# Kernel optimization log

Hardware: AMD Instinct MI355X
Metric: run time of the kernel (lower is better)

## Reference

```python
import jax, jax.numpy as jnp
import numpy as np

N_NODES = 100000
N_EDGES = 3200000  # avg degree 32
NFEAT = 512
NOUT = 7
DIMS = [NFEAT, 12, 10, 8, 6, 4, NOUT]  # hard-coded hidden widths from __init__


def setup_inputs() -> dict:
    key = jax.random.key(0)
    ks = jax.random.split(key, 4 + 2 * 6)
    inp = {
        "x": jax.random.normal(ks[0], (N_NODES, NFEAT), dtype=jnp.float32),
        "edge_val": jax.random.uniform(ks[1], (N_EDGES,), dtype=jnp.float32) / 32.0,  # ~normalized adj
        "edge_src": jax.random.randint(ks[2], (N_EDGES,), 0, N_NODES),
        "edge_dst": jax.random.randint(ks[3], (N_EDGES,), 0, N_NODES),
    }
    for i in range(6):
        s = 1.0 / np.sqrt(DIMS[i + 1])  # pygcn reset_parameters: U(-1/sqrt(out), 1/sqrt(out))
        inp[f"W{i+1}"] = jax.random.uniform(ks[4 + 2 * i], (DIMS[i], DIMS[i + 1]), jnp.float32, -s, s)
        inp[f"b{i+1}"] = jax.random.uniform(ks[5 + 2 * i], (DIMS[i + 1],), jnp.float32, -s, s)
    return inp


def reference(x, edge_val, W1, b1, W2, b2, W3, b3, W4, b4, W5, b5, W6, b6,
              edge_src, edge_dst):
    n = x.shape[0]

    def gc(h, W, b):
        s = h @ W                                   # [N, out] dense mm
        m = edge_val[:, None] * s[edge_src]         # gather + scale per edge
        agg = jax.ops.segment_sum(m, edge_dst, num_segments=n)  # spmm scatter
        return agg + b

    tanhshrink = lambda v: v - jnp.tanh(v)

    h = gc(x, W1, b1)                # dropout p=0 -> identity
    h = jax.nn.relu(gc(h, W2, b2))   # eval-mode dropout -> identity
    h = tanhshrink(gc(h, W3, b3))
    h = tanhshrink(gc(h, W4, b4))
    h = gc(h, W5, b5)
    return gc(h, W6, b6)
```

## Files before the change

### kernel.cpp

```cpp
#include <hip/hip_runtime.h>
#include <hip/hip_bf16.h>
#include <math.h>
#include <stdint.h>


#define T_EDGES 12800
#define NB_MAX  1600
#define FCAP    2560

__global__ __launch_bounds__(256) void hist_kernel(const int* __restrict__ dst,
                                                   int* __restrict__ ghist, int E, int NB) {
    __shared__ int h[NB_MAX];
    for (int i = threadIdx.x; i < NB; i += 256) h[i] = 0;
    __syncthreads();
    int base = blockIdx.x * T_EDGES;
    int n = min(T_EDGES, E - base);
    for (int i = threadIdx.x; i < n; i += 256)
        atomicAdd(&h[((unsigned)dst[base + i]) >> 6], 1);
    __syncthreads();
    for (int i = threadIdx.x; i < NB; i += 256)
        ghist[(size_t)blockIdx.x * NB + i] = h[i];
}

__global__ __launch_bounds__(256) void scanA_kernel(const int* __restrict__ ghist,
                                                    int* __restrict__ btot, int NT, int NB) {
    __shared__ int red[256];
    int b = blockIdx.x, t = threadIdx.x;
    int s = 0;
    for (int tt = t; tt < NT; tt += 256) s += ghist[(size_t)tt * NB + b];
    red[t] = s;
    __syncthreads();
    for (int off = 128; off > 0; off >>= 1) {
        if (t < off) red[t] += red[t + off];
        __syncthreads();
    }
    if (t == 0) btot[b] = red[0];
}

__global__ __launch_bounds__(256) void scanB_kernel(const int* __restrict__ btot,
                                                    int* __restrict__ bbase,
                                                    int* __restrict__ bucket_ptr, int NB) {
    __shared__ int part[256];
    int t = threadIdx.x;
    int chunk = (NB + 255) / 256;
    int lo = t * chunk, hi = min(lo + chunk, NB);
    int s = 0;
    for (int i = lo; i < hi; i++) s += btot[i];
    part[t] = s;
    __syncthreads();
    for (int off = 1; off < 256; off <<= 1) {
        int x = (t >= off) ? part[t - off] : 0;
        __syncthreads();
        part[t] += x;
        __syncthreads();
    }
    int run = part[t] - s;
    for (int i = lo; i < hi; i++) {
        bbase[i] = run;
        bucket_ptr[i] = run;
        run += btot[i];
    }
    if (t == 255) bucket_ptr[NB] = run;
}

__global__ __launch_bounds__(256) void scanC_kernel(const int* __restrict__ ghist,
                                                    const int* __restrict__ bbase,
                                                    int* __restrict__ goff, int NT, int NB) {
    __shared__ int part[256];
    int b = blockIdx.x, t = threadIdx.x;
    int v = (t < NT) ? ghist[(size_t)t * NB + b] : 0;
    part[t] = v;
    __syncthreads();
    for (int off = 1; off < 256; off <<= 1) {
        int x = (t >= off) ? part[t - off] : 0;
        __syncthreads();
        part[t] += x;
        __syncthreads();
    }
    if (t < NT) goff[(size_t)t * NB + b] = bbase[b] + part[t] - v;
}

__global__ __launch_bounds__(256) void scatter_kernel(const int* __restrict__ src,
                                                      const int* __restrict__ dst,
                                                      const float* __restrict__ val,
                                                      const int* __restrict__ ghist,
                                                      const int* __restrict__ goff,
                                                      int2* __restrict__ edges, int E, int NB) {
    __shared__ unsigned perm[T_EDGES];
    __shared__ int loff[NB_MAX];
    __shared__ int lcur[NB_MAX];
    __shared__ int part[256];
    int tb = blockIdx.x, t = threadIdx.x;
    int base = tb * T_EDGES;
    int n = min(T_EDGES, E - base);

    int chunk = (NB + 255) / 256;
    int lo = t * chunk, hi = min(lo + chunk, NB);
    int s = 0;
    for (int i = lo; i < hi; i++) {
        int c = ghist[(size_t)tb * NB + i];
        loff[i] = c;
        s += c;
    }
    part[t] = s;
    __syncthreads();
    for (int off = 1; off < 256; off <<= 1) {
        int x = (t >= off) ? part[t - off] : 0;
        __syncthreads();
        part[t] += x;
        __syncthreads();
    }
    int run = part[t] - s;
    for (int i = lo; i < hi; i++) {
        int c = loff[i];
        loff[i] = run;
        lcur[i] = run;
        run += c;
    }
    __syncthreads();

    for (int i = t; i < n; i += 256) {
        int d = dst[base + i];
        unsigned b = ((unsigned)d) >> 6;
        int p = atomicAdd(&lcur[b], 1);
        perm[p] = (unsigned)i | (b << 14) | ((unsigned)(d & 63) << 25);
    }
    __syncthreads();

    for (int o = t; o < n; o += 256) {
        unsigned v = perm[o];
        int li = v & 16383;
        int b  = (v >> 14) & 2047;
        int ld = v >> 25;
        int g  = goff[(size_t)tb * NB + b] + (o - loff[b]);
        edges[g] = make_int2(src[base + li] | (ld << 17), __float_as_int(val[base + li]));
    }
}

__global__ __launch_bounds__(256) void finalize_kernel(int2* __restrict__ edges,
                                                       const int* __restrict__ bucket_ptr) {
    __shared__ int2 recs[FCAP];
    __shared__ int2 recs2[FCAP];
    __shared__ int cnt[64], offs[64], cur[64];
    int b = blockIdx.x, t = threadIdx.x;
    int s0 = bucket_ptr[b], s1 = bucket_ptr[b + 1];
    int ne = min(s1 - s0, FCAP);
    if (t < 64) cnt[t] = 0;
    __syncthreads();
    for (int i = t; i < ne; i += 256) {
        int2 r = edges[s0 + i];
        recs[i] = r;
        atomicAdd(&cnt[(r.x >> 17) & 63], 1);
    }
    __syncthreads();
    if (t == 0) {
        int run = 0;
        for (int i = 0; i < 64; i++) { offs[i] = run; run += cnt[i]; }
    }
    __syncthreads();
    if (t < 64) cur[t] = offs[t];
    __syncthreads();
    for (int i = t; i < ne; i += 256) {
        int2 r = recs[i];
        int ld = (r.x >> 17) & 63;
        int p = atomicAdd(&cur[ld], 1);
        recs2[p] = r;
    }
    __syncthreads();
    for (int i = t; i < ne; i += 256) edges[s0 + i] = recs2[i];
}

__global__ __launch_bounds__(256) void dense1_kernel(const float* __restrict__ x,
                                                     const float* __restrict__ W,
                                                     float* __restrict__ out, int N) {
    __shared__ float xs[256 * 33];
    const int t    = threadIdx.x;
    const int row0 = blockIdx.x * 256;
    const int r    = row0 + t;

    float acc[12];
#pragma unroll
    for (int j = 0; j < 12; j++) acc[j] = 0.f;

    for (int tile = 0; tile < 16; ++tile) {
#pragma unroll
        for (int i = 0; i < 8; i++) {
            int idx4 = t + 256 * i;
            int flat = idx4 * 4;
            int rl   = flat >> 5;
            int c    = flat & 31;
            int rg   = row0 + rl;
            if (rg >= N) rg = N - 1;
            const float4 v = *(const float4*)(x + (size_t)rg * 512 + tile * 32 + c);
            float* p = &xs[rl * 33 + c];
            p[0] = v.x; p[1] = v.y; p[2] = v.z; p[3] = v.w;
        }
        __syncthreads();
#pragma unroll 8
        for (int kk = 0; kk < 32; ++kk) {
            float xv = xs[t * 33 + kk];
            int k = tile * 32 + kk;
#pragma unroll
            for (int j = 0; j < 12; j++) acc[j] += xv * W[k * 12 + j];
        }
        __syncthreads();
    }
    if (r < N) {
#pragma unroll
        for (int j = 0; j < 12; j++) out[(size_t)r * 12 + j] = acc[j];
    }
}

template <int NV, int DIN, int DOUT, int OSTR, int ACT, bool FINAL>
__global__ __launch_bounds__(256) void layer_kernel(const int2* __restrict__ edges,
                                                    const int* __restrict__ bucket_ptr,
                                                    const float* __restrict__ s,
                                                    const float* __restrict__ bias,
                                                    const float* __restrict__ W,
                                                    float* __restrict__ out, int N) {
    constexpr int ASTR = 13;
    __shared__ int2  ebuf[FCAP];
    __shared__ float acc[64 * ASTR];
    const int b = blockIdx.x, t = threadIdx.x;
    const int s0 = bucket_ptr[b];
    const int ne = min(bucket_ptr[b + 1] - s0, FCAP);

    for (int i = t; i < 64 * ASTR; i += 256) acc[i] = 0.f;
    for (int i = t; i < ne; i += 256) ebuf[i] = edges[s0 + i];
    __syncthreads();

    const int K  = (ne + 255) >> 8;
    const int i0 = t * K;
    const int i1 = min(i0 + K, ne);
    if (i0 < i1) {
        const float4* sv = (const float4*)s;
        float4 a[NV];
#pragma unroll
        for (int v = 0; v < NV; v++) a[v] = make_float4(0.f, 0.f, 0.f, 0.f);
        int cd = (ebuf[i0].x >> 17) & 63;
        for (int i = i0; i < i1; ++i) {
            int2 ev = ebuf[i];
            int ld = (ev.x >> 17) & 63;
            if (ld != cd) {
#pragma unroll
                for (int v = 0; v < NV; v++) {
                    atomicAdd(&acc[cd * ASTR + 4 * v + 0], a[v].x);
                    atomicAdd(&acc[cd * ASTR + 4 * v + 1], a[v].y);
                    atomicAdd(&acc[cd * ASTR + 4 * v + 2], a[v].z);
                    atomicAdd(&acc[cd * ASTR + 4 * v + 3], a[v].w);
                    a[v] = make_float4(0.f, 0.f, 0.f, 0.f);
                }
                cd = ld;
            }
            float w = __int_as_float(ev.y);
            const float4* srow = sv + (size_t)(ev.x & 0x1FFFF) * NV;
#pragma unroll
            for (int v = 0; v < NV; v++) {
                float4 xr = srow[v];
                a[v].x += w * xr.x; a[v].y += w * xr.y;
                a[v].z += w * xr.z; a[v].w += w * xr.w;
            }
        }
#pragma unroll
        for (int v = 0; v < NV; v++) {
            atomicAdd(&acc[cd * ASTR + 4 * v + 0], a[v].x);
            atomicAdd(&acc[cd * ASTR + 4 * v + 1], a[v].y);
            atomicAdd(&acc[cd * ASTR + 4 * v + 2], a[v].z);
            atomicAdd(&acc[cd * ASTR + 4 * v + 3], a[v].w);
        }
    }
    __syncthreads();

    if (t < 64) {
        int node = (b << 6) + t;
        if (node < N) {
            float h[DIN];
#pragma unroll
            for (int k = 0; k < DIN; k++) {
                float z = acc[t * ASTR + k] + bias[k];
                if (ACT == 1) z = fmaxf(z, 0.f);
                else if (ACT == 2) z = z - tanhf(z);
                h[k] = z;
            }
            if (FINAL) {
#pragma unroll
                for (int k = 0; k < DIN; k++) out[(size_t)node * DIN + k] = h[k];
            } else {
                float o[OSTR];
#pragma unroll
                for (int j = 0; j < OSTR; j++) o[j] = 0.f;
#pragma unroll
                for (int j = 0; j < DOUT; j++) {
                    float tj = 0.f;
#pragma unroll
                    for (int k = 0; k < DIN; k++) tj += h[k] * W[k * DOUT + j];
                    o[j] = tj;
                }
                float4* orow = (float4*)(out + (size_t)node * OSTR);
#pragma unroll
                for (int v = 0; v < OSTR / 4; v++)
                    orow[v] = make_float4(o[4 * v], o[4 * v + 1], o[4 * v + 2], o[4 * v + 3]);
            }
        }
    }
}


static inline size_t align256(size_t x) { return (x + 255) & ~(size_t)255; }

extern "C" void kernel_launch(void* const* d_in, const int* in_sizes, int n_in,
                              void* d_out, int out_size, void* d_ws, size_t ws_size,
                              hipStream_t stream) {
    const float* x        = (const float*)d_in[0];
    const float* edge_val = (const float*)d_in[1];
    const int*   edge_src = (const int*)d_in[2];
    const int*   edge_dst = (const int*)d_in[3];
    const float* W1 = (const float*)d_in[4];   const float* b1 = (const float*)d_in[5];
    const float* W2 = (const float*)d_in[6];   const float* b2 = (const float*)d_in[7];
    const float* W3 = (const float*)d_in[8];   const float* b3 = (const float*)d_in[9];
    const float* W4 = (const float*)d_in[10];  const float* b4 = (const float*)d_in[11];
    const float* W5 = (const float*)d_in[12];  const float* b5 = (const float*)d_in[13];
    const float* W6 = (const float*)d_in[14];  const float* b6 = (const float*)d_in[15];

    const int N = in_sizes[0] / 512;
    const int E = in_sizes[1];
    float* out = (float*)d_out;

    const int NB = (N + 63) >> 6;
    const int NT = (E + T_EDGES - 1) / T_EDGES;
    const int nb = (N + 255) / 256;

    char* w = (char*)d_ws;
    float* A          = (float*)w;  w += align256((size_t)N * 12 * sizeof(float));
    float* B          = (float*)w;  w += align256((size_t)N * 12 * sizeof(float));
    int*   ghist      = (int*)w;    w += align256((size_t)NT * NB * sizeof(int));
    int*   goff       = (int*)w;    w += align256((size_t)NT * NB * sizeof(int));
    int*   btot       = (int*)w;    w += align256((size_t)NB * sizeof(int));
    int*   bbase      = (int*)w;    w += align256((size_t)NB * sizeof(int));
    int*   bucket_ptr = (int*)w;    w += align256((size_t)(NB + 1) * sizeof(int));
    int2*  edges      = (int2*)w;   w += align256((size_t)E * sizeof(int2));

    hist_kernel<<<NT, 256, 0, stream>>>(edge_dst, ghist, E, NB);
    scanA_kernel<<<NB, 256, 0, stream>>>(ghist, btot, NT, NB);
    scanB_kernel<<<1, 256, 0, stream>>>(btot, bbase, bucket_ptr, NB);
    scanC_kernel<<<NB, 256, 0, stream>>>(ghist, bbase, goff, NT, NB);
    scatter_kernel<<<NT, 256, 0, stream>>>(edge_src, edge_dst, edge_val, ghist, goff, edges, E, NB);
    finalize_kernel<<<NB, 256, 0, stream>>>(edges, bucket_ptr);

    dense1_kernel<<<nb, 256, 0, stream>>>(x, W1, A, N);

    layer_kernel<3, 12, 10, 12, 0, false><<<NB, 256, 0, stream>>>(edges, bucket_ptr, A, b1, W2, B, N);
    layer_kernel<3, 10, 8, 8, 1, false><<<NB, 256, 0, stream>>>(edges, bucket_ptr, B, b2, W3, A, N);
    layer_kernel<2, 8, 6, 8, 2, false><<<NB, 256, 0, stream>>>(edges, bucket_ptr, A, b3, W4, B, N);
    layer_kernel<2, 6, 4, 4, 2, false><<<NB, 256, 0, stream>>>(edges, bucket_ptr, B, b4, W5, A, N);
    layer_kernel<1, 4, 7, 8, 0, false><<<NB, 256, 0, stream>>>(edges, bucket_ptr, A, b5, W6, B, N);
    layer_kernel<2, 7, 7, 8, 0, true><<<NB, 256, 0, stream>>>(edges, bucket_ptr, B, b6, (const float*)nullptr, out, N);
}
```

Before: 744.8 us.

## Fuse layer chain into persistent kernel with grid barriers and fixed-capacity buckets

```diff
diff --git a/kernel.cpp b/kernel.cpp
--- a/kernel.cpp
+++ b/kernel.cpp
@@ -1,5 +1,4 @@
 #include <hip/hip_runtime.h>
-#include <hip/hip_bf16.h>
 #include <math.h>
 #include <stdint.h>
 
@@ -7,11 +6,16 @@
 #define T_EDGES 12800
 #define NB_MAX  1600
 #define FCAP    2560
+#define KPT     10
+#define ASTR    13
+#define CHAIN_GRID 768
 
 __global__ __launch_bounds__(256) void hist_kernel(const int* __restrict__ dst,
-                                                   int* __restrict__ ghist, int E, int NB) {
+                                                   int* __restrict__ ghist,
+                                                   int* __restrict__ gbar, int E, int NB) {
     __shared__ int h[NB_MAX];
     for (int i = threadIdx.x; i < NB; i += 256) h[i] = 0;
+    if (blockIdx.x == 0 && threadIdx.x < 32) atomicExch(&gbar[threadIdx.x], 0);
     __syncthreads();
     int base = blockIdx.x * T_EDGES;
     int n = min(T_EDGES, E - base);
@@ -22,50 +26,9 @@
         ghist[(size_t)blockIdx.x * NB + i] = h[i];
 }
 
-__global__ __launch_bounds__(256) void scanA_kernel(const int* __restrict__ ghist,
+__global__ __launch_bounds__(256) void scanC_kernel(const int* __restrict__ ghist,
+                                                    int* __restrict__ goff,
                                                     int* __restrict__ btot, int NT, int NB) {
-    __shared__ int red[256];
-    int b = blockIdx.x, t = threadIdx.x;
-    int s = 0;
-    for (int tt = t; tt < NT; tt += 256) s += ghist[(size_t)tt * NB + b];
-    red[t] = s;
-    __syncthreads();
-    for (int off = 128; off > 0; off >>= 1) {
-        if (t < off) red[t] += red[t + off];
-        __syncthreads();
-    }
-    if (t == 0) btot[b] = red[0];
-}
-
-__global__ __launch_bounds__(256) void scanB_kernel(const int* __restrict__ btot,
-                                                    int* __restrict__ bbase,
-                                                    int* __restrict__ bucket_ptr, int NB) {
-    __shared__ int part[256];
-    int t = threadIdx.x;
-    int chunk = (NB + 255) / 256;
-    int lo = t * chunk, hi = min(lo + chunk, NB);
-    int s = 0;
-    for (int i = lo; i < hi; i++) s += btot[i];
-    part[t] = s;
-    __syncthreads();
-    for (int off = 1; off < 256; off <<= 1) {
-        int x = (t >= off) ? part[t - off] : 0;
-        __syncthreads();
-        part[t] += x;
-        __syncthreads();
-    }
-    int run = part[t] - s;
-    for (int i = lo; i < hi; i++) {
-        bbase[i] = run;
-        bucket_ptr[i] = run;
-        run += btot[i];
-    }
-    if (t == 255) bucket_ptr[NB] = run;
-}
-
-__global__ __launch_bounds__(256) void scanC_kernel(const int* __restrict__ ghist,
-                                                    const int* __restrict__ bbase,
-                                                    int* __restrict__ goff, int NT, int NB) {
     __shared__ int part[256];
     int b = blockIdx.x, t = threadIdx.x;
     int v = (t < NT) ? ghist[(size_t)t * NB + b] : 0;
@@ -77,7 +40,8 @@
         part[t] += x;
         __syncthreads();
     }
-    if (t < NT) goff[(size_t)t * NB + b] = bbase[b] + part[t] - v;
+    if (t < NT) goff[(size_t)t * NB + b] = b * FCAP + part[t] - v;
+    if (t == 255) btot[b] = part[255];
 }
 
 __global__ __launch_bounds__(256) void scatter_kernel(const int* __restrict__ src,
@@ -138,13 +102,13 @@
 }
 
 __global__ __launch_bounds__(256) void finalize_kernel(int2* __restrict__ edges,
-                                                       const int* __restrict__ bucket_ptr) {
+                                                       const int* __restrict__ btot) {
     __shared__ int2 recs[FCAP];
     __shared__ int2 recs2[FCAP];
     __shared__ int cnt[64], offs[64], cur[64];
     int b = blockIdx.x, t = threadIdx.x;
-    int s0 = bucket_ptr[b], s1 = bucket_ptr[b + 1];
-    int ne = min(s1 - s0, FCAP);
+    size_t s0 = (size_t)b * FCAP;
+    int ne = min(btot[b], FCAP);
     if (t < 64) cnt[t] = 0;
     __syncthreads();
     for (int i = t; i < ne; i += 256) {
@@ -168,6 +132,8 @@
     }
     __syncthreads();
     for (int i = t; i < ne; i += 256) edges[s0 + i] = recs2[i];
+    for (int i = ne + t; i < FCAP; i += 256)
+        edges[s0 + i] = make_int2(63 << 17, 0);
 }
 
 __global__ __launch_bounds__(256) void dense1_kernel(const float* __restrict__ x,
@@ -211,54 +177,70 @@
     }
 }
 
+__device__ __forceinline__ void gsync(int* ctr, int nblk) {
+    __syncthreads();
+    if (threadIdx.x == 0) {
+        __threadfence();
+        atomicAdd(ctr, 1);
+        int spins = 0;
+        while (__hip_atomic_load(ctr, __ATOMIC_RELAXED, __HIP_MEMORY_SCOPE_AGENT) < nblk) {
+            __builtin_amdgcn_s_sleep(8);
+            if (++spins > (1 << 22)) break;
+        }
+    }
+    __syncthreads();
+    __threadfence();
+}
+
 template <int NV, int DIN, int DOUT, int OSTR, int ACT, bool FINAL>
-__global__ __launch_bounds__(256) void layer_kernel(const int2* __restrict__ edges,
-                                                    const int* __restrict__ bucket_ptr,
-                                                    const float* __restrict__ s,
-                                                    const float* __restrict__ bias,
-                                                    const float* __restrict__ W,
-                                                    float* __restrict__ out, int N) {
-    constexpr int ASTR = 13;
-    __shared__ int2  ebuf[FCAP];
-    __shared__ float acc[64 * ASTR];
-    const int b = blockIdx.x, t = threadIdx.x;
-    const int s0 = bucket_ptr[b];
-    const int ne = min(bucket_ptr[b + 1] - s0, FCAP);
-
+__device__ __forceinline__ void layer_body(int b, const int2* __restrict__ edges,
+                                           const float* __restrict__ s,
+                                           const float* __restrict__ bias,
+                                           const float* __restrict__ W,
+                                           float* __restrict__ out, int N,
+                                           float* acc) {
+    const int t = threadIdx.x;
     for (int i = t; i < 64 * ASTR; i += 256) acc[i] = 0.f;
-    for (int i = t; i < ne; i += 256) ebuf[i] = edges[s0 + i];
-    __syncthreads();
-
-    const int K  = (ne + 255) >> 8;
-    const int i0 = t * K;
-    const int i1 = min(i0 + K, ne);
-    if (i0 < i1) {
+    __syncthreads();
+
+    {
+        const int4* ep = (const int4*)(edges + (size_t)b * FCAP) + t * (KPT / 2);
+        int4 e[KPT / 2];
+#pragma unroll
+        for (int q = 0; q < KPT / 2; q++) e[q] = ep[q];
+
         const float4* sv = (const float4*)s;
         float4 a[NV];
 #pragma unroll
         for (int v = 0; v < NV; v++) a[v] = make_float4(0.f, 0.f, 0.f, 0.f);
-        int cd = (ebuf[i0].x >> 17) & 63;
-        for (int i = i0; i < i1; ++i) {
-            int2 ev = ebuf[i];
-            int ld = (ev.x >> 17) & 63;
-            if (ld != cd) {
+        int cd = (e[0].x >> 17) & 63;
+
+#pragma unroll
+        for (int q = 0; q < KPT / 2; q++) {
+#pragma unroll
+            for (int half = 0; half < 2; half++) {
+                int ex = half ? e[q].z : e[q].x;
+                int ey = half ? e[q].w : e[q].y;
+                int ld = (ex >> 17) & 63;
+                if (ld != cd) {
+#pragma unroll
+                    for (int v = 0; v < NV; v++) {
+                        atomicAdd(&acc[cd * ASTR + 4 * v + 0], a[v].x);
+                        atomicAdd(&acc[cd * ASTR + 4 * v + 1], a[v].y);
+                        atomicAdd(&acc[cd * ASTR + 4 * v + 2], a[v].z);
+                        atomicAdd(&acc[cd * ASTR + 4 * v + 3], a[v].w);
+                        a[v] = make_float4(0.f, 0.f, 0.f, 0.f);
+                    }
+                    cd = ld;
+                }
+                float w = __int_as_float(ey);
+                const float4* srow = sv + (size_t)(ex & 0x1FFFF) * NV;
 #pragma unroll
                 for (int v = 0; v < NV; v++) {
-                    atomicAdd(&acc[cd * ASTR + 4 * v + 0], a[v].x);
-                    atomicAdd(&acc[cd * ASTR + 4 * v + 1], a[v].y);
-                    atomicAdd(&acc[cd * ASTR + 4 * v + 2], a[v].z);
-                    atomicAdd(&acc[cd * ASTR + 4 * v + 3], a[v].w);
-                    a[v] = make_float4(0.f, 0.f, 0.f, 0.f);
+                    float4 xr = srow[v];
+                    a[v].x += w * xr.x; a[v].y += w * xr.y;
+                    a[v].z += w * xr.z; a[v].w += w * xr.w;
                 }
-                cd = ld;
-            }
-            float w = __int_as_float(ev.y);
-            const float4* srow = sv + (size_t)(ev.x & 0x1FFFF) * NV;
-#pragma unroll
-            for (int v = 0; v < NV; v++) {
-                float4 xr = srow[v];
-                a[v].x += w * xr.x; a[v].y += w * xr.y;
-                a[v].z += w * xr.z; a[v].w += w * xr.w;
             }
         }
 #pragma unroll
@@ -303,6 +285,38 @@
             }
         }
     }
+    __syncthreads();
+}
+
+__global__ __launch_bounds__(256, 3) void chain_kernel(
+    const int2* __restrict__ edges, float* __restrict__ A, float* __restrict__ B,
+    const float* __restrict__ b1, const float* __restrict__ W2,
+    const float* __restrict__ b2, const float* __restrict__ W3,
+    const float* __restrict__ b3, const float* __restrict__ W4,
+    const float* __restrict__ b4, const float* __restrict__ W5,
+    const float* __restrict__ b5, const float* __restrict__ W6,
+    const float* __restrict__ b6, float* __restrict__ out,
+    int N, int NB, int* __restrict__ gbar) {
+    __shared__ float acc[64 * ASTR];
+    const int g = gridDim.x;
+
+    for (int b = blockIdx.x; b < NB; b += g)
+        layer_body<3, 12, 10, 12, 0, false>(b, edges, A, b1, W2, B, N, acc);
+    gsync(&gbar[0], g);
+    for (int b = blockIdx.x; b < NB; b += g)
+        layer_body<3, 10, 8, 8, 1, false>(b, edges, B, b2, W3, A, N, acc);
+    gsync(&gbar[1], g);
+    for (int b = blockIdx.x; b < NB; b += g)
+        layer_body<2, 8, 6, 8, 2, false>(b, edges, A, b3, W4, B, N, acc);
+    gsync(&gbar[2], g);
+    for (int b = blockIdx.x; b < NB; b += g)
+        layer_body<2, 6, 4, 4, 2, false>(b, edges, B, b4, W5, A, N, acc);
+    gsync(&gbar[3], g);
+    for (int b = blockIdx.x; b < NB; b += g)
+        layer_body<1, 4, 7, 8, 0, false>(b, edges, A, b5, W6, B, N, acc);
+    gsync(&gbar[4], g);
+    for (int b = blockIdx.x; b < NB; b += g)
+        layer_body<2, 7, 7, 8, 0, true>(b, edges, B, b6, (const float*)nullptr, out, N, acc);
 }
 
 
@@ -331,28 +345,21 @@
     const int nb = (N + 255) / 256;
 
     char* w = (char*)d_ws;
-    float* A          = (float*)w;  w += align256((size_t)N * 12 * sizeof(float));
-    float* B          = (float*)w;  w += align256((size_t)N * 12 * sizeof(float));
-    int*   ghist      = (int*)w;    w += align256((size_t)NT * NB * sizeof(int));
-    int*   goff       = (int*)w;    w += align256((size_t)NT * NB * sizeof(int));
-    int*   btot       = (int*)w;    w += align256((size_t)NB * sizeof(int));
-    int*   bbase      = (int*)w;    w += align256((size_t)NB * sizeof(int));
-    int*   bucket_ptr = (int*)w;    w += align256((size_t)(NB + 1) * sizeof(int));
-    int2*  edges      = (int2*)w;   w += align256((size_t)E * sizeof(int2));
-
-    hist_kernel<<<NT, 256, 0, stream>>>(edge_dst, ghist, E, NB);
-    scanA_kernel<<<NB, 256, 0, stream>>>(ghist, btot, NT, NB);
-    scanB_kernel<<<1, 256, 0, stream>>>(btot, bbase, bucket_ptr, NB);
-    scanC_kernel<<<NB, 256, 0, stream>>>(ghist, bbase, goff, NT, NB);
+    float* A     = (float*)w;  w += align256((size_t)N * 12 * sizeof(float));
+    float* B     = (float*)w;  w += align256((size_t)N * 12 * sizeof(float));
+    int*   ghist = (int*)w;    w += align256((size_t)NT * NB * sizeof(int));
+    int*   goff  = (int*)w;    w += align256((size_t)NT * NB * sizeof(int));
+    int*   btot  = (int*)w;    w += align256((size_t)NB * sizeof(int));
+    int*   gbar  = (int*)w;    w += align256(32 * sizeof(int));
+    int2*  edges = (int2*)w;   w += align256((size_t)NB * FCAP * sizeof(int2));
+
+    hist_kernel<<<NT, 256, 0, stream>>>(edge_dst, ghist, gbar, E, NB);
+    scanC_kernel<<<NB, 256, 0, stream>>>(ghist, goff, btot, NT, NB);
     scatter_kernel<<<NT, 256, 0, stream>>>(edge_src, edge_dst, edge_val, ghist, goff, edges, E, NB);
-    finalize_kernel<<<NB, 256, 0, stream>>>(edges, bucket_ptr);
+    finalize_kernel<<<NB, 256, 0, stream>>>(edges, btot);
 
     dense1_kernel<<<nb, 256, 0, stream>>>(x, W1, A, N);
 
-    layer_kernel<3, 12, 10, 12, 0, false><<<NB, 256, 0, stream>>>(edges, bucket_ptr, A, b1, W2, B, N);
-    layer_kernel<3, 10, 8, 8, 1, false><<<NB, 256, 0, stream>>>(edges, bucket_ptr, B, b2, W3, A, N);
-    layer_kernel<2, 8, 6, 8, 2, false><<<NB, 256, 0, stream>>>(edges, bucket_ptr, A, b3, W4, B, N);
-    layer_kernel<2, 6, 4, 4, 2, false><<<NB, 256, 0, stream>>>(edges, bucket_ptr, B, b4, W5, A, N);
-    layer_kernel<1, 4, 7, 8, 0, false><<<NB, 256, 0, stream>>>(edges, bucket_ptr, A, b5, W6, B, N);
-    layer_kernel<2, 7, 7, 8, 0, true><<<NB, 256, 0, stream>>>(edges, bucket_ptr, B, b6, (const float*)nullptr, out, N);
-}
+    chain_kernel<<<CHAIN_GRID, 256, 0, stream>>>(edges, A, B, b1, W2, b2, W3, b3, W4,
+                                                 b4, W5, b5, W6, b6, out, N, NB, gbar);
+}
```

After: 1.337 ms. 79.5% more time.
